# Optimization experiments

Measured on AMD Instinct MI355X. Metric: run time of the kernel, lower is better.

## Reference

```python
import jax, jax.numpy as jnp
import numpy as np


def setup_inputs() -> dict:
    key = jax.random.key(0)
    k1, k2 = jax.random.split(key)
    x = jax.random.normal(k1, (8, 4096, 256), dtype=jnp.float32)
    embed = jax.random.normal(k2, (1, 8192, 256), dtype=jnp.float32)
    return {"x": x, "embed": embed}


def reference(x, embed):
    # EuclideanCodebook.forward, eval mode, sample_codebook_temp=0.
    # x: [b, n, d]  (ndim < 4 -> a leading codebook dim h=1 is added)
    # embed: [h, c, d]
    xf = x.astype(jnp.float32)[None]              # [h, b, n, d]
    h, b, n, d = xf.shape
    flatten = xf.reshape(h, b * n, d)             # [h, N, d]

    # dist = -cdist(flatten, embed, p=2)
    x2 = jnp.sum(flatten * flatten, axis=-1, keepdims=True)   # [h, N, 1]
    e2 = jnp.sum(embed * embed, axis=-1)                      # [h, c]
    xe = jnp.einsum('hnd,hcd->hnc', flatten, embed)           # [h, N, c]
    d2 = jnp.maximum(x2 + e2[:, None, :] - 2.0 * xe, 0.0)
    dist = -jnp.sqrt(d2)                                      # [h, N, c]

    # gumbel_sample with temperature == 0  ->  argmax
    embed_ind = jnp.argmax(dist, axis=-1)                     # [h, N]
    embed_ind = embed_ind.reshape(h, b, n)                    # [h, b, n]

    # batched_embedding: gather codes per codebook
    quantize = jax.vmap(lambda e, i: e[i])(embed, embed_ind)  # [h, b, n, d]

    # needs_codebook_dim -> squeeze leading h
    return quantize[0], embed_ind[0]
```

## Files before the change

### kernel.cpp

```cpp
#include <hip/hip_runtime.h>
#include <math.h>

#define D       256
#define NROWS   32768
#define CODES   8192
#define QOFF    8388608

#define BM      256
#define BN      256
#define NSPL    2
#define SPLC    (CODES / NSPL)
#define NCHUNK  (SPLC / BN)
#define NSTEP   (NCHUNK * 4)
#define NBLK    256
#define LQ      2048

#define MARG_COEF 0.016f
#define MARG_ABS  0.10f

#define OFF_AH    0ull
#define OFF_X2    16777216ull
#define OFF_NX    16908288ull
#define OFF_E2    17039360ull
#define OFF_RM    17072128ull
#define OFF_PK    17203200ull
#define OFF_MISC  17465344ull
#define OFF_BCNT  17465600ull
#define OFF_CAND  17469696ull
#define WS_NEED3  30052608ull

typedef __attribute__((ext_vector_type(8)))  short bf16x8;
typedef __attribute__((ext_vector_type(16))) float f32x16;

__device__ __forceinline__ int SWK(int b) { return b ^ (((b >> 7) & 7) << 4); }

__device__ __forceinline__ void gload16(const void* g, void* l) {
  __builtin_amdgcn_global_load_lds(
      (const __attribute__((address_space(1))) unsigned int*)g,
      (__attribute__((address_space(3))) unsigned int*)l, 16, 0, 0);
}

__device__ __forceinline__ unsigned short bf16rn(float x) {
  unsigned u = __float_as_uint(x);
  return (unsigned short)((u + 0x7fffu + ((u >> 16) & 1u)) >> 16);
}

__device__ __forceinline__ unsigned encf(float f) {
  unsigned b = __float_as_uint(f);
  return (b >> 31) ? ~b : (b | 0x80000000u);
}
__device__ __forceinline__ float decf(unsigned u) {
  return __uint_as_float((u >> 31) ? (u ^ 0x80000000u) : ~u);
}

__global__ __launch_bounds__(256) void init_kernel(unsigned* __restrict__ misc,
                                                   unsigned* __restrict__ rowMinU,
                                                   unsigned long long* __restrict__ pKey) {
  int i = blockIdx.x * 256 + threadIdx.x;
  if (i < 16) misc[i] = 0u;
  rowMinU[i] = 0xFFFFFFFFu;
  pKey[i] = ~0ull;
}

__global__ __launch_bounds__(256) void prep_kernel(const float* __restrict__ x,
                                                   const float* __restrict__ embed,
                                                   unsigned short* __restrict__ A_h,
                                                   unsigned short* __restrict__ E_h,
                                                   float* __restrict__ x2,
                                                   float* __restrict__ nx,
                                                   float* __restrict__ e2,
                                                   unsigned* __restrict__ misc) {
  int wid  = threadIdx.x >> 6;
  int lane = threadIdx.x & 63;
  int rid  = blockIdx.x * 4 + wid;
  const float* src;
  unsigned short* dst;
  if (rid < NROWS) { src = x + (size_t)rid * D;               dst = A_h + (size_t)rid * D; }
  else             { src = embed + (size_t)(rid - NROWS) * D; dst = E_h + (size_t)(rid - NROWS) * D; }
  float4 v = *(const float4*)(src + lane * 4);
  ushort4 hv = make_ushort4(bf16rn(v.x), bf16rn(v.y), bf16rn(v.z), bf16rn(v.w));
  *(ushort4*)(dst + lane * 4) = hv;
  float p = v.x * v.x + v.y * v.y + v.z * v.z + v.w * v.w;
  #pragma unroll
  for (int off = 32; off > 0; off >>= 1) p += __shfl_down(p, off);
  if (lane == 0) {
    float n = sqrtf(p);
    if (rid < NROWS) { x2[rid] = p; nx[rid] = n; }
    else { e2[rid - NROWS] = p; atomicMax(&misc[2], __float_as_uint(n)); }
  }
}

template<int MODE>
__global__ __launch_bounds__(512, 2) void gemm_pass(
    const unsigned short* __restrict__ A_h,
    const unsigned short* __restrict__ E_h,
    const float* __restrict__ e2g,
    const float* __restrict__ nxg,
    const unsigned* __restrict__ miscR,
    unsigned* __restrict__ rowMinU,
    unsigned* __restrict__ cand,
    unsigned* __restrict__ blkCnt,
    unsigned* __restrict__ ovCnt,
    unsigned OVCAP) {
  __shared__ __align__(16) char As0[32768];
  __shared__ __align__(16) char As1[32768];
  __shared__ __align__(16) char Bs0[32768];
  __shared__ __align__(16) char Bs1[32768];
  __shared__ unsigned lbuf[MODE ? LQ : 1];
  __shared__ unsigned lcnt;

  const int tid  = threadIdx.x;
  const int lane = tid & 63;
  const int wave = tid >> 6;
  const int wm = wave >> 1;
  const int wn = wave & 1;
  const int l31 = lane & 31;
  const int hi16 = (lane >> 5) << 4;
  const int lh4  = (lane >> 5) << 2;
  const int rowBase = blockIdx.x * BM;
  const int split   = blockIdx.y;
  const int seg     = blockIdx.y * 128 + blockIdx.x;

  const int Ccom = hi16 ^ ((l31 & 7) << 4);
  const int Aoff = (wm * 64 + l31) << 7;
  const int Boff = (wn * 128 + l31) << 7;

  int stRow[4], stCo[4], stDst[4];
  #pragma unroll
  for (int i = 0; i < 4; i++) {
    int q = i * 512 + tid;
    int u = SWK(q << 4);
    stRow[i] = u >> 7;
    stCo[i]  = u & 127;
    stDst[i] = (q & ~63) << 4;
  }

  auto STAGE = [&](char* Ad, char* Bd, int s) {
    int cc = s >> 2, kb = s & 3;
    const int cBase = split * SPLC + cc * BN;
    #pragma unroll
    for (int i = 0; i < 4; i++) {
      gload16((const char*)A_h + (((size_t)(rowBase + stRow[i])) << 9) + (kb << 7) + stCo[i],
              Ad + stDst[i]);
      gload16((const char*)E_h + (((size_t)(cBase + stRow[i])) << 9) + (kb << 7) + stCo[i],
              Bd + stDst[i]);
    }
  };

  STAGE(As0, Bs0, 0);
  if (MODE == 1 && tid == 0) lcnt = 0;

  float state[2][16];
  if (MODE == 0) {
    #pragma unroll
    for (int fm = 0; fm < 2; fm++)
      #pragma unroll
      for (int rg = 0; rg < 16; rg++) state[fm][rg] = INFINITY;
  } else {
    float neMaxF = __uint_as_float(miscR[2]);
    #pragma unroll
    for (int fm = 0; fm < 2; fm++)
      #pragma unroll
      for (int rg = 0; rg < 16; rg++) {
        int row = rowBase + wm * 64 + fm * 32 + ((rg & 3) + 8 * (rg >> 2)) + lh4;
        state[fm][rg] = decf(rowMinU[row]) + fmaf(MARG_COEF * nxg[row], neMaxF, MARG_ABS);
      }
  }

  f32x16 acc[2][4];
  #pragma unroll
  for (int i = 0; i < 2; i++)
    #pragma unroll
    for (int j = 0; j < 4; j++) acc[i][j] = (f32x16)(0.0f);

  __syncthreads();

  for (int s = 0; s < NSTEP; ++s) {
    char* Ac = (s & 1) ? As1 : As0;
    char* Bc = (s & 1) ? Bs1 : Bs0;
    if (s + 1 < NSTEP) STAGE((s & 1) ? As0 : As1, (s & 1) ? Bs0 : Bs1, s + 1);

    #pragma unroll
    for (int ks = 0; ks < 4; ++ks) {
      const int off = Ccom ^ (ks << 5);
      bf16x8 a0 = *(const bf16x8*)(Ac + Aoff + off);
      bf16x8 a1 = *(const bf16x8*)(Ac + Aoff + 4096 + off);
      bf16x8 b0 = *(const bf16x8*)(Bc + Boff + off);
      bf16x8 b1 = *(const bf16x8*)(Bc + Boff + 4096 + off);
      bf16x8 b2 = *(const bf16x8*)(Bc + Boff + 8192 + off);
      bf16x8 b3 = *(const bf16x8*)(Bc + Boff + 12288 + off);
      acc[0][0] = __builtin_amdgcn_mfma_f32_32x32x16_bf16(a0, b0, acc[0][0], 0, 0, 0);
      acc[1][0] = __builtin_amdgcn_mfma_f32_32x32x16_bf16(a1, b0, acc[1][0], 0, 0, 0);
      acc[0][1] = __builtin_amdgcn_mfma_f32_32x32x16_bf16(a0, b1, acc[0][1], 0, 0, 0);
      acc[1][1] = __builtin_amdgcn_mfma_f32_32x32x16_bf16(a1, b1, acc[1][1], 0, 0, 0);
      acc[0][2] = __builtin_amdgcn_mfma_f32_32x32x16_bf16(a0, b2, acc[0][2], 0, 0, 0);
      acc[1][2] = __builtin_amdgcn_mfma_f32_32x32x16_bf16(a1, b2, acc[1][2], 0, 0, 0);
      acc[0][3] = __builtin_amdgcn_mfma_f32_32x32x16_bf16(a0, b3, acc[0][3], 0, 0, 0);
      acc[1][3] = __builtin_amdgcn_mfma_f32_32x32x16_bf16(a1, b3, acc[1][3], 0, 0, 0);
    }

    if ((s & 3) == 3) {
      const int cc = s >> 2;
      const int cBase = split * SPLC + cc * BN;
      if (MODE == 0) {
        #pragma unroll
        for (int g = 0; g < 4; g++) {
          float e2c = e2g[cBase + wn * 128 + g * 32 + l31];
          #pragma unroll
          for (int fm = 0; fm < 2; fm++)
            #pragma unroll
            for (int rg = 0; rg < 16; rg++)
              state[fm][rg] = fminf(state[fm][rg], fmaf(acc[fm][g][rg], -2.0f, e2c));
        }
      } else {
        #pragma unroll
        for (int g = 0; g < 4; g++) {
          int col = cBase + wn * 128 + g * 32 + l31;
          float e2c = e2g[col];
          #pragma unroll
          for (int fm = 0; fm < 2; fm++)
            #pragma unroll
            for (int rg = 0; rg < 16; rg++) {
              float q = fmaf(acc[fm][g][rg], -2.0f, e2c);
              if (q <= state[fm][rg]) {
                int row = rowBase + wm * 64 + fm * 32 + ((rg & 3) + 8 * (rg >> 2)) + lh4;
                unsigned en = (unsigned)((row << 13) | col);
                unsigned p = atomicAdd(&lcnt, 1u);
                if (p < LQ) lbuf[p] = en;
                else { unsigned gp = atomicAdd(ovCnt, 1u);
                       if (gp < OVCAP) cand[(size_t)NBLK * LQ + gp] = en; }
              }
            }
        }
      }
      #pragma unroll
      for (int i = 0; i < 2; i++)
        #pragma unroll
        for (int j = 0; j < 4; j++) acc[i][j] = (f32x16)(0.0f);
    }

    __syncthreads();
  }

  if (MODE == 0) {
    #pragma unroll
    for (int fm = 0; fm < 2; fm++)
      #pragma unroll
      for (int rg = 0; rg < 16; rg++) {
        float v = state[fm][rg];
        #pragma unroll
        for (int off = 1; off < 32; off <<= 1) v = fminf(v, __shfl_xor(v, off));
        if (l31 == 0) {
          int row = rowBase + wm * 64 + fm * 32 + ((rg & 3) + 8 * (rg >> 2)) + lh4;
          atomicMin(&rowMinU[row], encf(v));
        }
      }
  } else {
    unsigned n = lcnt; if (n > LQ) n = LQ;
    for (unsigned i = tid; i < n; i += 512) cand[(size_t)seg * LQ + i] = lbuf[i];
    if (tid == 0) blkCnt[seg] = n;
  }
}

__global__ __launch_bounds__(256) void refine_kernel(const float* __restrict__ x,
                                                     const float* __restrict__ embed,
                                                     const float* __restrict__ x2g,
                                                     const float* __restrict__ e2g,
                                                     const unsigned* __restrict__ blkCnt,
                                                     const unsigned* __restrict__ cand,
                                                     const unsigned* __restrict__ miscR,
                                                     unsigned long long* __restrict__ pKey,
                                                     unsigned OVCAP) {
  const int tid = threadIdx.x;
  const int l16 = tid & 15;
  const int gid = tid >> 4;

  auto doItem = [&](unsigned pk) {
    int row = (int)(pk >> 13), col = (int)(pk & 8191u);
    double s = 0.0;
    #pragma unroll
    for (int p = 0; p < 4; p++) {
      float4 xv = *(const float4*)&x[(size_t)row * D + p * 64 + l16 * 4];
      float4 ev = *(const float4*)&embed[(size_t)col * D + p * 64 + l16 * 4];
      s = fma((double)xv.x, (double)ev.x, s);
      s = fma((double)xv.y, (double)ev.y, s);
      s = fma((double)xv.z, (double)ev.z, s);
      s = fma((double)xv.w, (double)ev.w, s);
    }
    #pragma unroll
    for (int off = 1; off < 16; off <<= 1) s += __shfl_xor(s, off);
    if (l16 == 0) {
      float xef = (float)s;
      float ss  = __fadd_rn(x2g[row], e2g[col]);
      float d2  = __fsub_rn(ss, __fmul_rn(2.0f, xef));
      d2 = fmaxf(d2, 0.0f);
      float sq = sqrtf(d2);
      unsigned long long key =
          ((unsigned long long)__float_as_uint(sq) << 32) | (unsigned)col;
      atomicMin(pKey + row, key);
    }
  };

  unsigned seg = blockIdx.x;
  unsigned n = blkCnt[seg]; if (n > LQ) n = LQ;
  const unsigned* segp = cand + (size_t)seg * LQ;
  for (unsigned i = gid; i < n; i += 16) doItem(segp[i]);

  unsigned ov = miscR[1]; if (ov > OVCAP) ov = OVCAP;
  const unsigned* ovp = cand + (size_t)NBLK * LQ;
  for (unsigned i = blockIdx.x * 16 + gid; i < ov; i += NBLK * 16) doItem(ovp[i]);
}

__global__ __launch_bounds__(256) void final_kernel(const float* __restrict__ embed,
                                                    const unsigned long long* __restrict__ pKey,
                                                    float* __restrict__ outQ,
                                                    float* __restrict__ indF) {
  int wid  = threadIdx.x >> 6;
  int lane = threadIdx.x & 63;
  int row  = blockIdx.x * 4 + wid;
  unsigned long long k = pKey[row];
  int idx = (int)(k & 8191ull);
  float4 v = *(const float4*)&embed[(size_t)idx * D + lane * 4];
  *(float4*)&outQ[(size_t)row * D + lane * 4] = v;
  if (lane == 0) indF[row] = (float)idx;
}

#define BM_F 128
#define BN_F 128
#define BK_F 32
#define NSPLIT_F 4
#define SPLIT_CF (CODES / NSPLIT_F)

__global__ __launch_bounds__(256) void sq_kernel(const float* __restrict__ x,
                                                 const float* __restrict__ embed,
                                                 float* __restrict__ x2,
                                                 float* __restrict__ e2) {
  int wid  = threadIdx.x >> 6;
  int lane = threadIdx.x & 63;
  int rid  = blockIdx.x * 4 + wid;
  const float* base = (rid < NROWS) ? (x + (size_t)rid * D)
                                    : (embed + (size_t)(rid - NROWS) * D);
  float4 v = *(const float4*)(base + lane * 4);
  float p = v.x * v.x + v.y * v.y + v.z * v.z + v.w * v.w;
  #pragma unroll
  for (int off = 32; off > 0; off >>= 1) p += __shfl_down(p, off);
  if (lane == 0) {
    if (rid < NROWS) x2[rid] = p;
    else             e2[rid - NROWS] = p;
  }
}

__global__ __launch_bounds__(256) void argmin_f32_kernel(const float* __restrict__ x,
                                                         const float* __restrict__ embed,
                                                         const float* __restrict__ x2,
                                                         const float* __restrict__ e2,
                                                         float* __restrict__ pVal,
                                                         int* __restrict__ pIdx) {
  __shared__ float As[BK_F][BM_F];
  __shared__ float Bs[BK_F][BN_F];
  const int tid = threadIdx.x;
  const int ty = tid >> 4, tx = tid & 15;
  const int rowBase = blockIdx.x * BM_F;
  const int split = blockIdx.y;
  const int r0 = ty * 8, c0 = tx * 8;
  float bestV[8]; int bestI[8];
  #pragma unroll
  for (int i = 0; i < 8; i++) { bestV[i] = -INFINITY; bestI[i] = 0; }
  float x2r[8];
  #pragma unroll
  for (int i = 0; i < 8; i++) x2r[i] = x2[rowBase + r0 + i];
  for (int chunk = 0; chunk < SPLIT_CF / BN_F; ++chunk) {
    const int cBase = split * SPLIT_CF + chunk * BN_F;
    float acc[8][8];
    #pragma unroll
    for (int i = 0; i < 8; i++)
      #pragma unroll
      for (int j = 0; j < 8; j++) acc[i][j] = 0.0f;
    for (int kb = 0; kb < D / BK_F; ++kb) {
      #pragma unroll
      for (int i = 0; i < 4; i++) {
        int f4 = tid + i * 256;
        int rr = f4 >> 3, k4 = f4 & 7;
        float4 va = *(const float4*)&x[(size_t)(rowBase + rr) * D + kb * BK_F + k4 * 4];
        As[k4 * 4 + 0][rr] = va.x; As[k4 * 4 + 1][rr] = va.y;
        As[k4 * 4 + 2][rr] = va.z; As[k4 * 4 + 3][rr] = va.w;
        float4 vb = *(const float4*)&embed[(size_t)(cBase + rr) * D + kb * BK_F + k4 * 4];
        Bs[k4 * 4 + 0][rr] = vb.x; Bs[k4 * 4 + 1][rr] = vb.y;
        Bs[k4 * 4 + 2][rr] = vb.z; Bs[k4 * 4 + 3][rr] = vb.w;
      }
      __syncthreads();
      #pragma unroll 8
      for (int kk = 0; kk < BK_F; kk++) {
        float a[8], b[8];
        *(float4*)&a[0] = *(const float4*)&As[kk][r0];
        *(float4*)&a[4] = *(const float4*)&As[kk][r0 + 4];
        *(float4*)&b[0] = *(const float4*)&Bs[kk][c0];
        *(float4*)&b[4] = *(const float4*)&Bs[kk][c0 + 4];
        #pragma unroll
        for (int i = 0; i < 8; i++)
          #pragma unroll
          for (int j = 0; j < 8; j++)
            acc[i][j] = fmaf(a[i], b[j], acc[i][j]);
      }
      __syncthreads();
    }
    #pragma unroll
    for (int j = 0; j < 8; j++) {
      int c = cBase + c0 + j;
      float e2c = e2[c];
      #pragma unroll
      for (int i = 0; i < 8; i++) {
        float s  = __fadd_rn(x2r[i], e2c);
        float u  = __fmul_rn(2.0f, acc[i][j]);
        float d2 = fmaxf(__fsub_rn(s, u), 0.0f);
        float dist = -sqrtf(d2);
        if (dist > bestV[i]) { bestV[i] = dist; bestI[i] = c; }
      }
    }
  }
  __syncthreads();
  float* Vl = &As[0][0];
  int*   Il = (int*)&Bs[0][0];
  #pragma unroll
  for (int i = 0; i < 8; i++) {
    Vl[(ty * 16 + tx) * 8 + i] = bestV[i];
    Il[(ty * 16 + tx) * 8 + i] = bestI[i];
  }
  __syncthreads();
  if (tid < BM_F) {
    int rr = tid, tyr = rr >> 3, ii = rr & 7;
    float bv = -INFINITY; int bi = 0;
    #pragma unroll
    for (int t = 0; t < 16; t++) {
      float v = Vl[(tyr * 16 + t) * 8 + ii];
      int  iv = Il[(tyr * 16 + t) * 8 + ii];
      if (v > bv || (v == bv && iv < bi)) { bv = v; bi = iv; }
    }
    pVal[split * NROWS + rowBase + rr] = bv;
    pIdx[split * NROWS + rowBase + rr] = bi;
  }
}

__global__ __launch_bounds__(256) void merge_f32_kernel(const float* __restrict__ pVal,
                                                        const int* __restrict__ pIdx,
                                                        float* __restrict__ indF) {
  int row = blockIdx.x * 256 + threadIdx.x;
  if (row >= NROWS) return;
  float bv = -INFINITY; int bi = 0;
  #pragma unroll
  for (int s = 0; s < NSPLIT_F; s++) {
    float v = pVal[s * NROWS + row];
    int  iv = pIdx[s * NROWS + row];
    if (v > bv || (v == bv && iv < bi)) { bv = v; bi = iv; }
  }
  indF[row] = (float)bi;
}

__global__ __launch_bounds__(256) void gather_f32_kernel(const float* __restrict__ embed,
                                                         const float* __restrict__ indF,
                                                         float* __restrict__ outQ) {
  int wid = threadIdx.x >> 6, lane = threadIdx.x & 63;
  int row = blockIdx.x * 4 + wid;
  int idx = (int)indF[row];
  float4 v = *(const float4*)&embed[(size_t)idx * D + lane * 4];
  *(float4*)&outQ[(size_t)row * D + lane * 4] = v;
}

extern "C" void kernel_launch(void* const* d_in, const int* in_sizes, int n_in,
                              void* d_out, int out_size, void* d_ws, size_t ws_size,
                              hipStream_t stream) {
  const float* x     = (const float*)d_in[0];
  const float* embed = (const float*)d_in[1];
  float* o = (float*)d_out;

  if (ws_size >= WS_NEED3) {
    char* w = (char*)d_ws;
    unsigned short* A_h = (unsigned short*)(w + OFF_AH);
    float* x2 = (float*)(w + OFF_X2);
    float* nx = (float*)(w + OFF_NX);
    float* e2 = (float*)(w + OFF_E2);
    unsigned* rowMinU = (unsigned*)(w + OFF_RM);
    unsigned long long* pKey = (unsigned long long*)(w + OFF_PK);
    unsigned* misc = (unsigned*)(w + OFF_MISC);
    unsigned* blkCnt = (unsigned*)(w + OFF_BCNT);
    unsigned* cand = (unsigned*)(w + OFF_CAND);
    unsigned capN  = (unsigned)((ws_size - OFF_CAND) / 4ull);
    unsigned OVCAP = capN - (unsigned)(NBLK * LQ);

    unsigned short* E_h = (unsigned short*)o;
    float* indF = o + QOFF;

    init_kernel<<<128, 256, 0, stream>>>(misc, rowMinU, pKey);
    prep_kernel<<<(NROWS + CODES) / 4, 256, 0, stream>>>(x, embed, A_h, E_h, x2, nx, e2, misc);
    dim3 gridC(NROWS / BM, NSPL);
    gemm_pass<0><<<gridC, 512, 0, stream>>>(A_h, E_h, e2, nx, misc, rowMinU,
                                            cand, blkCnt, &misc[1], OVCAP);
    gemm_pass<1><<<gridC, 512, 0, stream>>>(A_h, E_h, e2, nx, misc, rowMinU,
                                            cand, blkCnt, &misc[1], OVCAP);
    refine_kernel<<<NBLK, 256, 0, stream>>>(x, embed, x2, e2, blkCnt, cand, misc,
                                            pKey, OVCAP);
    final_kernel<<<NROWS / 4, 256, 0, stream>>>(embed, pKey, o, indF);
  } else {
    float* x2   = o;
    float* e2   = o + 32768;
    float* pVal = o + 65536;
    int*   pIdx = (int*)(o + 196608);
    float* indF = o + QOFF;
    sq_kernel<<<(NROWS + CODES) / 4, 256, 0, stream>>>(x, embed, x2, e2);
    dim3 gridB(NROWS / BM_F, NSPLIT_F);
    argmin_f32_kernel<<<gridB, 256, 0, stream>>>(x, embed, x2, e2, pVal, pIdx);
    merge_f32_kernel<<<NROWS / 256, 256, 0, stream>>>(pVal, pIdx, indF);
    gather_f32_kernel<<<NROWS / 4, 256, 0, stream>>>(embed, indF, o);
  }
}
```

Before: 444.4 us.

## Fuse two GEMM passes into one with running-min candidate emission and filter

Replaces the two full bf16 GEMM passes (first computing row minima, second emitting candidates within a margin) with a single pass. That pass warms up on the first code chunk, keeps a running per-row minimum, and emits candidates with their coarse score against the running bound. A new filter kernel then prunes candidates against the final global row minimum before the fp64 refine, which now runs over a flat list with more blocks. This roughly halves the MFMA work, in exchange for recomputing one chunk, extra cross-lane reductions per chunk, more candidate traffic, and larger fixed-capacity workspace buffers that could overflow.

```diff
diff --git a/kernel.cpp b/kernel.cpp
--- a/kernel.cpp
+++ b/kernel.cpp
@@ -11,9 +11,13 @@
 #define NSPL    2
 #define SPLC    (CODES / NSPL)
 #define NCHUNK  (SPLC / BN)
-#define NSTEP   (NCHUNK * 4)
+#define NT      (NCHUNK + 1)
+#define NSTEP   (NT * 4)
 #define NBLK    256
 #define LQ      2048
+#define SEGQ    12288u
+#define OVCAP   262144u
+#define CAP2    1048576u
 
 #define MARG_COEF 0.016f
 #define MARG_ABS  0.10f
@@ -26,8 +30,9 @@
 #define OFF_PK    17203200ull
 #define OFF_MISC  17465344ull
 #define OFF_BCNT  17465600ull
-#define OFF_CAND  17469696ull
-#define WS_NEED3  30052608ull
+#define OFF_L2    17469696ull
+#define OFF_CAND  21664000ull
+#define WS_NEED   48926976ull
 
 typedef __attribute__((ext_vector_type(8)))  short bf16x8;
 typedef __attribute__((ext_vector_type(16))) float f32x16;
@@ -90,24 +95,22 @@
   }
 }
 
-template<int MODE>
-__global__ __launch_bounds__(512, 2) void gemm_pass(
+__global__ __launch_bounds__(512, 2) void gemm_coarse(
     const unsigned short* __restrict__ A_h,
     const unsigned short* __restrict__ E_h,
     const float* __restrict__ e2g,
     const float* __restrict__ nxg,
     const unsigned* __restrict__ miscR,
     unsigned* __restrict__ rowMinU,
-    unsigned* __restrict__ cand,
+    uint2* __restrict__ cand,
     unsigned* __restrict__ blkCnt,
-    unsigned* __restrict__ ovCnt,
-    unsigned OVCAP) {
+    unsigned* __restrict__ ovCnt) {
   __shared__ __align__(16) char As0[32768];
   __shared__ __align__(16) char As1[32768];
   __shared__ __align__(16) char Bs0[32768];
   __shared__ __align__(16) char Bs1[32768];
-  __shared__ unsigned lbuf[MODE ? LQ : 1];
-  __shared__ unsigned lcnt;
+  __shared__ uint2 lbuf[LQ];
+  __shared__ unsigned lcnt, lnS, lbaseS;
 
   const int tid  = threadIdx.x;
   const int lane = tid & 63;
@@ -136,7 +139,8 @@
   }
 
   auto STAGE = [&](char* Ad, char* Bd, int s) {
-    int cc = s >> 2, kb = s & 3;
+    int t = s >> 2, kb = s & 3;
+    int cc = t ? (t - 1) : 0;
     const int cBase = split * SPLC + cc * BN;
     #pragma unroll
     for (int i = 0; i < 4; i++) {
@@ -147,25 +151,20 @@
     }
   };
 
+  if (tid == 0) lcnt = 0;
+  const float neMaxF = __uint_as_float(miscR[2]);
+  float runm[2][16], rowC[2][16];
+  #pragma unroll
+  for (int fm = 0; fm < 2; fm++)
+    #pragma unroll
+    for (int rg = 0; rg < 16; rg++) {
+      int row = rowBase + wm * 64 + fm * 32 + ((rg & 3) + 8 * (rg >> 2)) + lh4;
+      rowC[fm][rg] = fmaf(MARG_COEF * nxg[row], neMaxF, MARG_ABS);
+      runm[fm][rg] = INFINITY;
+    }
+  unsigned segOff = 0;
+
   STAGE(As0, Bs0, 0);
-  if (MODE == 1 && tid == 0) lcnt = 0;
-
-  float state[2][16];
-  if (MODE == 0) {
-    #pragma unroll
-    for (int fm = 0; fm < 2; fm++)
-      #pragma unroll
-      for (int rg = 0; rg < 16; rg++) state[fm][rg] = INFINITY;
-  } else {
-    float neMaxF = __uint_as_float(miscR[2]);
-    #pragma unroll
-    for (int fm = 0; fm < 2; fm++)
-      #pragma unroll
-      for (int rg = 0; rg < 16; rg++) {
-        int row = rowBase + wm * 64 + fm * 32 + ((rg & 3) + 8 * (rg >> 2)) + lh4;
-        state[fm][rg] = decf(rowMinU[row]) + fmaf(MARG_COEF * nxg[row], neMaxF, MARG_ABS);
-      }
-  }
 
   f32x16 acc[2][4];
   #pragma unroll
@@ -199,36 +198,47 @@
       acc[1][3] = __builtin_amdgcn_mfma_f32_32x32x16_bf16(a1, b3, acc[1][3], 0, 0, 0);
     }
 
+    const int t = s >> 2;
     if ((s & 3) == 3) {
-      const int cc = s >> 2;
+      const int cc = t ? (t - 1) : 0;
       const int cBase = split * SPLC + cc * BN;
-      if (MODE == 0) {
+      float e2r[4];
+      #pragma unroll
+      for (int g = 0; g < 4; g++) e2r[g] = e2g[cBase + wn * 128 + g * 32 + l31];
+
+      #pragma unroll
+      for (int g = 0; g < 4; g++)
         #pragma unroll
-        for (int g = 0; g < 4; g++) {
-          float e2c = e2g[cBase + wn * 128 + g * 32 + l31];
+        for (int fm = 0; fm < 2; fm++)
           #pragma unroll
-          for (int fm = 0; fm < 2; fm++)
-            #pragma unroll
-            for (int rg = 0; rg < 16; rg++)
-              state[fm][rg] = fminf(state[fm][rg], fmaf(acc[fm][g][rg], -2.0f, e2c));
+          for (int rg = 0; rg < 16; rg++)
+            runm[fm][rg] = fminf(runm[fm][rg], fmaf(acc[fm][g][rg], -2.0f, e2r[g]));
+      #pragma unroll
+      for (int fm = 0; fm < 2; fm++)
+        #pragma unroll
+        for (int rg = 0; rg < 16; rg++) {
+          float v = runm[fm][rg];
+          #pragma unroll
+          for (int off = 1; off < 32; off <<= 1) v = fminf(v, __shfl_xor(v, off));
+          runm[fm][rg] = v;
         }
-      } else {
+
+      if (t >= 1) {
         #pragma unroll
         for (int g = 0; g < 4; g++) {
           int col = cBase + wn * 128 + g * 32 + l31;
-          float e2c = e2g[col];
           #pragma unroll
           for (int fm = 0; fm < 2; fm++)
             #pragma unroll
             for (int rg = 0; rg < 16; rg++) {
-              float q = fmaf(acc[fm][g][rg], -2.0f, e2c);
-              if (q <= state[fm][rg]) {
+              float q = fmaf(acc[fm][g][rg], -2.0f, e2r[g]);
+              if (q <= runm[fm][rg] + rowC[fm][rg]) {
                 int row = rowBase + wm * 64 + fm * 32 + ((rg & 3) + 8 * (rg >> 2)) + lh4;
-                unsigned en = (unsigned)((row << 13) | col);
+                uint2 en = make_uint2((unsigned)((row << 13) | col), __float_as_uint(q));
                 unsigned p = atomicAdd(&lcnt, 1u);
                 if (p < LQ) lbuf[p] = en;
                 else { unsigned gp = atomicAdd(ovCnt, 1u);
-                       if (gp < OVCAP) cand[(size_t)NBLK * LQ + gp] = en; }
+                       if (gp < OVCAP) cand[(size_t)NBLK * SEGQ + gp] = en; }
               }
             }
         }
@@ -240,42 +250,75 @@
     }
 
     __syncthreads();
-  }
-
-  if (MODE == 0) {
+
+    if ((s & 3) == 3 && t >= 1) {
+      if (tid == 0) {
+        unsigned n = lcnt; if (n > LQ) n = LQ;
+        lnS = n; lbaseS = segOff; segOff += n; lcnt = 0;
+      }
+      __syncthreads();
+      unsigned n = lnS, base = lbaseS;
+      for (unsigned i = tid; i < n; i += 512) {
+        unsigned gp = base + i;
+        if (gp < SEGQ) cand[(size_t)seg * SEGQ + gp] = lbuf[i];
+        else { unsigned op = atomicAdd(ovCnt, 1u);
+               if (op < OVCAP) cand[(size_t)NBLK * SEGQ + op] = lbuf[i]; }
+      }
+    }
+  }
+
+  if (l31 == 0) {
     #pragma unroll
     for (int fm = 0; fm < 2; fm++)
       #pragma unroll
       for (int rg = 0; rg < 16; rg++) {
-        float v = state[fm][rg];
-        #pragma unroll
-        for (int off = 1; off < 32; off <<= 1) v = fminf(v, __shfl_xor(v, off));
-        if (l31 == 0) {
-          int row = rowBase + wm * 64 + fm * 32 + ((rg & 3) + 8 * (rg >> 2)) + lh4;
-          atomicMin(&rowMinU[row], encf(v));
-        }
-      }
-  } else {
-    unsigned n = lcnt; if (n > LQ) n = LQ;
-    for (unsigned i = tid; i < n; i += 512) cand[(size_t)seg * LQ + i] = lbuf[i];
-    if (tid == 0) blkCnt[seg] = n;
-  }
+        int row = rowBase + wm * 64 + fm * 32 + ((rg & 3) + 8 * (rg >> 2)) + lh4;
+        atomicMin(&rowMinU[row], encf(runm[fm][rg]));
+      }
+  }
+  if (tid == 0) blkCnt[seg] = (segOff > SEGQ) ? SEGQ : segOff;
+}
+
+__global__ __launch_bounds__(256) void filter_kernel(const uint2* __restrict__ cand,
+                                                     const unsigned* __restrict__ blkCnt,
+                                                     unsigned* __restrict__ misc,
+                                                     const unsigned* __restrict__ rowMinU,
+                                                     const float* __restrict__ nxg,
+                                                     unsigned* __restrict__ list2) {
+  const float neMaxF = __uint_as_float(misc[2]);
+  auto test = [&](uint2 en) {
+    unsigned row = en.x >> 13;
+    float q  = __uint_as_float(en.y);
+    float rm = decf(rowMinU[row]);
+    float rc = fmaf(MARG_COEF * nxg[row], neMaxF, MARG_ABS);
+    if (q <= rm + rc) {
+      unsigned p = atomicAdd(&misc[3], 1u);
+      if (p < CAP2) list2[p] = en.x;
+    }
+  };
+  unsigned seg = blockIdx.x;
+  unsigned n = blkCnt[seg]; if (n > SEGQ) n = SEGQ;
+  const uint2* sp = cand + (size_t)seg * SEGQ;
+  for (unsigned i = threadIdx.x; i < n; i += 256) test(sp[i]);
+
+  unsigned ov = misc[1]; if (ov > OVCAP) ov = OVCAP;
+  const uint2* op = cand + (size_t)NBLK * SEGQ;
+  for (unsigned i = blockIdx.x * 256 + threadIdx.x; i < ov; i += NBLK * 256) test(op[i]);
 }
 
 __global__ __launch_bounds__(256) void refine_kernel(const float* __restrict__ x,
                                                      const float* __restrict__ embed,
                                                      const float* __restrict__ x2g,
                                                      const float* __restrict__ e2g,
-                                                     const unsigned* __restrict__ blkCnt,
-                                                     const unsigned* __restrict__ cand,
                                                      const unsigned* __restrict__ miscR,
-                                                     unsigned long long* __restrict__ pKey,
-                                                     unsigned OVCAP) {
-  const int tid = threadIdx.x;
-  const int l16 = tid & 15;
-  const int gid = tid >> 4;
-
-  auto doItem = [&](unsigned pk) {
+                                                     const unsigned* __restrict__ list2,
+                                                     unsigned long long* __restrict__ pKey) {
+  const int l16 = threadIdx.x & 15;
+  unsigned total = miscR[3]; if (total > CAP2) total = CAP2;
+  unsigned gid = (blockIdx.x * 256 + threadIdx.x) >> 4;
+  unsigned ng  = (gridDim.x * 256) >> 4;
+  for (unsigned i = gid; i < total; i += ng) {
+    unsigned pk = list2[i];
     int row = (int)(pk >> 13), col = (int)(pk & 8191u);
     double s = 0.0;
     #pragma unroll
@@ -299,16 +342,7 @@
           ((unsigned long long)__float_as_uint(sq) << 32) | (unsigned)col;
       atomicMin(pKey + row, key);
     }
-  };
-
-  unsigned seg = blockIdx.x;
-  unsigned n = blkCnt[seg]; if (n > LQ) n = LQ;
-  const unsigned* segp = cand + (size_t)seg * LQ;
-  for (unsigned i = gid; i < n; i += 16) doItem(segp[i]);
-
-  unsigned ov = miscR[1]; if (ov > OVCAP) ov = OVCAP;
-  const unsigned* ovp = cand + (size_t)NBLK * LQ;
-  for (unsigned i = blockIdx.x * 16 + gid; i < ov; i += NBLK * 16) doItem(ovp[i]);
+  }
 }
 
 __global__ __launch_bounds__(256) void final_kernel(const float* __restrict__ embed,
@@ -473,7 +507,7 @@
   const float* embed = (const float*)d_in[1];
   float* o = (float*)d_out;
 
-  if (ws_size >= WS_NEED3) {
+  if (ws_size >= WS_NEED) {
     char* w = (char*)d_ws;
     unsigned short* A_h = (unsigned short*)(w + OFF_AH);
     float* x2 = (float*)(w + OFF_X2);
@@ -483,9 +517,8 @@
     unsigned long long* pKey = (unsigned long long*)(w + OFF_PK);
     unsigned* misc = (unsigned*)(w + OFF_MISC);
     unsigned* blkCnt = (unsigned*)(w + OFF_BCNT);
-    unsigned* cand = (unsigned*)(w + OFF_CAND);
-    unsigned capN  = (unsigned)((ws_size - OFF_CAND) / 4ull);
-    unsigned OVCAP = capN - (unsigned)(NBLK * LQ);
+    unsigned* list2 = (unsigned*)(w + OFF_L2);
+    uint2* cand = (uint2*)(w + OFF_CAND);
 
     unsigned short* E_h = (unsigned short*)o;
     float* indF = o + QOFF;
@@ -493,12 +526,10 @@
     init_kernel<<<128, 256, 0, stream>>>(misc, rowMinU, pKey);
     prep_kernel<<<(NROWS + CODES) / 4, 256, 0, stream>>>(x, embed, A_h, E_h, x2, nx, e2, misc);
     dim3 gridC(NROWS / BM, NSPL);
-    gemm_pass<0><<<gridC, 512, 0, stream>>>(A_h, E_h, e2, nx, misc, rowMinU,
-                                            cand, blkCnt, &misc[1], OVCAP);
-    gemm_pass<1><<<gridC, 512, 0, stream>>>(A_h, E_h, e2, nx, misc, rowMinU,
-                                            cand, blkCnt, &misc[1], OVCAP);
-    refine_kernel<<<NBLK, 256, 0, stream>>>(x, embed, x2, e2, blkCnt, cand, misc,
-                                            pKey, OVCAP);
+    gemm_coarse<<<gridC, 512, 0, stream>>>(A_h, E_h, e2, nx, misc, rowMinU,
+                                           cand, blkCnt, &misc[1]);
+    filter_kernel<<<NBLK, 256, 0, stream>>>(cand, blkCnt, misc, rowMinU, nx, list2);
+    refine_kernel<<<1024, 256, 0, stream>>>(x, embed, x2, e2, misc, list2, pKey);
     final_kernel<<<NROWS / 4, 256, 0, stream>>>(embed, pKey, o, indF);
   } else {
     float* x2   = o;
```

New measurement: 1.163 ms. 2.62x slower.
